# Optimization experiments

Hardware: AMD Instinct MI355X
Metric: run time of the kernel (lower is better)

The kernel has to match this reference:

```python
import jax, jax.numpy as jnp
import numpy as np

N_QUBITS = 4
N_LAYERS = 2
BATCH = 1048576


def _rx(theta):
    # PennyLane RX(theta) = exp(-i theta X / 2)
    c = jnp.cos(theta / 2).astype(jnp.complex64)
    s = jnp.sin(theta / 2).astype(jnp.complex64)
    return jnp.stack([jnp.stack([c, -1j * s]), jnp.stack([-1j * s, c])])


def _rot(phi, theta, omega):
    # PennyLane Rot(phi, theta, omega) = RZ(omega) RY(theta) RZ(phi)
    ct = jnp.cos(theta / 2)
    st = jnp.sin(theta / 2)
    e1 = jnp.exp(-0.5j * (phi + omega))
    e2 = jnp.exp(0.5j * (phi - omega))
    e3 = jnp.exp(-0.5j * (phi - omega))
    e4 = jnp.exp(0.5j * (phi + omega))
    return jnp.stack([jnp.stack([e1 * ct, -e2 * st]),
                      jnp.stack([e3 * st, e4 * ct])]).astype(jnp.complex64)


def _apply_1q(psi, U, w):
    # psi: (2,)*N_QUBITS complex statevector; contract U on wire w
    psi = jnp.tensordot(U, psi, axes=([1], [w]))
    return jnp.moveaxis(psi, 0, w)


def _apply_cnot(psi, c, t):
    psi = jnp.moveaxis(psi, (c, t), (0, 1))
    psi = jnp.stack([psi[0], psi[1, ::-1]], axis=0)  # flip target where control=1
    return jnp.moveaxis(psi, (0, 1), (c, t))


def _circuit(x, weights):
    psi = jnp.zeros((2,) * N_QUBITS, jnp.complex64).at[(0,) * N_QUBITS].set(1.0)
    # AngleEmbedding: RX(x[i]) on each wire
    for w in range(N_QUBITS):
        psi = _apply_1q(psi, _rx(x[w]), w)
    # StronglyEntanglingLayers: Rot per wire, then CNOT ring with range r
    for l in range(N_LAYERS):
        for w in range(N_QUBITS):
            psi = _apply_1q(psi, _rot(weights[l, w, 0], weights[l, w, 1], weights[l, w, 2]), w)
        r = (l % (N_QUBITS - 1)) + 1  # default ranges in StronglyEntanglingLayers
        for w in range(N_QUBITS):
            psi = _apply_cnot(psi, w, (w + r) % N_QUBITS)
    probs = jnp.real(psi * jnp.conj(psi))
    sign = jnp.array([1.0, -1.0], jnp.float32)
    z = [jnp.sum(probs * sign.reshape([2 if a == i else 1 for a in range(N_QUBITS)]))
         for i in range(N_QUBITS)]
    return jnp.stack(z)  # <Z_i> for each wire, shape [4]


def setup_inputs() -> dict:
    key = jax.random.key(0)
    k1, k2, k3, k4 = jax.random.split(key, 4)
    noise = jax.random.normal(k1, (BATCH, N_QUBITS), dtype=jnp.float32)
    q_weights = jax.random.normal(k2, (N_LAYERS, N_QUBITS, 3), dtype=jnp.float32) * 0.1
    W = jax.random.normal(k3, (4, N_QUBITS), dtype=jnp.float32) * 0.5
    b = jax.random.normal(k4, (4,), dtype=jnp.float32) * 0.1
    return {"noise": noise, "q_weights": q_weights, "W": W, "b": b}


def reference(noise, q_weights, W, b):
    q_out = jax.vmap(lambda x: _circuit(x, q_weights))(noise)  # [B, 4] float32
    out = q_out @ W.T + b                                      # Linear(4, 4)
    energy = jnp.abs(out[:, 0]) + 0.001
    return jnp.concatenate([energy[:, None], out[:, 1:]], axis=1)
```

## Files before the change

kernel.cpp:

```cpp
#include <hip/hip_runtime.h>
#include <math.h>


__global__ __launch_bounds__(256) void qg_precompute(
    const float* __restrict__ qw,
    const float* __restrict__ Wm,
    const float* __restrict__ bv,
    float* __restrict__ Dcoef)
{
  __shared__ float  gm[24][8];
  __shared__ float2 Ul[16][16];
  __shared__ float  wj[4][16];
  __shared__ float2 A[4][16][16];
  const int tid = threadIdx.x;

  if (tid < 24) {
    const float phi = qw[tid*3 + 0];
    const float th  = qw[tid*3 + 1];
    const float om  = qw[tid*3 + 2];
    float st, ct, sa, ca, sd, cd;
    __sincosf(0.5f*th,       &st, &ct);
    __sincosf(0.5f*(phi+om), &sa, &ca);
    __sincosf(0.5f*(phi-om), &sd, &cd);
    gm[tid][0] =  ca*ct; gm[tid][1] = -sa*ct;
    gm[tid][2] = -cd*st; gm[tid][3] = -sd*st;
    gm[tid][4] =  cd*st; gm[tid][5] = -sd*st;
    gm[tid][6] =  ca*ct; gm[tid][7] =  sa*ct;
  }
  if (tid >= 192) {
    const int j = (tid - 192) >> 4, k = tid & 15;
    float s = 0.f;
    #pragma unroll
    for (int i = 0; i < 4; ++i)
      s += Wm[j*4 + i] * (((k >> (3 - i)) & 1) ? -1.f : 1.f);
    wj[j][k] = s;
  }
  __syncthreads();

  {
    const int col = tid >> 4, row = tid & 15;
    float vr = (row == col) ? 1.f : 0.f, vi = 0.f;
    #pragma unroll
    for (int l = 0; l < 2; ++l) {
      #pragma unroll
      for (int w = 0; w < 4; ++w) {
        const int g = l*4 + w;
        const float m00r = gm[g][0], m00i = gm[g][1];
        const float m01r = gm[g][2], m01i = gm[g][3];
        const float m10r = gm[g][4], m10i = gm[g][5];
        const float m11r = gm[g][6], m11i = gm[g][7];
        const int mask = 8 >> w;
        const float pr = __shfl_xor(vr, mask);
        const float pi = __shfl_xor(vi, mask);
        float nr, ni;
        if (!(row & mask)) {
          nr = m00r*vr - m00i*vi + m01r*pr - m01i*pi;
          ni = m00r*vi + m00i*vr + m01r*pi + m01i*pr;
        } else {
          nr = m10r*pr - m10i*pi + m11r*vr - m11i*vi;
          ni = m10r*pi + m10i*pr + m11r*vi + m11i*vr;
        }
        vr = nr; vi = ni;
      }
      const int r = l + 1;
      #pragma unroll
      for (int w = 0; w < 4; ++w) {
        const int t  = (w + r) & 3;
        const int cm = 8 >> w, tm = 8 >> t;
        const float pr = __shfl_xor(vr, tm);
        const float pi = __shfl_xor(vi, tm);
        if (row & cm) { vr = pr; vi = pi; }
      }
    }
    Ul[row][col] = make_float2(vr, vi);
  }
  __syncthreads();

  {
    const int s = tid >> 4, t = tid & 15;
    float ar[4] = {0,0,0,0}, ai[4] = {0,0,0,0};
    #pragma unroll
    for (int k = 0; k < 16; ++k) {
      const float2 us = Ul[k][s], ut = Ul[k][t];
      const float pr = us.x*ut.x + us.y*ut.y;
      const float pi = us.x*ut.y - us.y*ut.x;
      #pragma unroll
      for (int j = 0; j < 4; ++j) { ar[j] += wj[j][k]*pr; ai[j] += wj[j][k]*pi; }
    }
    #pragma unroll
    for (int j = 0; j < 4; ++j) A[j][s][t] = make_float2(ar[j], ai[j]);
  }
  __syncthreads();

  for (int item = tid; item < 324; item += 256) {
    const int j = item / 81, p = item % 81;
    const int p1 = p / 27, p2 = (p / 9) % 3, p3 = (p / 3) % 3, p4 = p % 3;
    int ym = 0, ny = 0;
    if (p1 == 2) { ym |= 8; ++ny; }
    if (p2 == 2) { ym |= 4; ++ny; }
    if (p3 == 2) { ym |= 2; ++ny; }
    if (p4 == 2) { ym |= 1; ++ny; }
    float sum = 0.f;
    for (int t = 0; t < 16; ++t) {
      const int t0 = (t>>3)&1, t1 = (t>>2)&1, t2 = (t>>1)&1, t3 = t&1;
      float sgn = 1.f;
      if      (p1 == 1) sgn *= t0 ? -1.f : 1.f;
      else if (p1 == 2) sgn *= t0 ?  1.f : -1.f;
      if      (p2 == 1) sgn *= t1 ? -1.f : 1.f;
      else if (p2 == 2) sgn *= t1 ?  1.f : -1.f;
      if      (p3 == 1) sgn *= t2 ? -1.f : 1.f;
      else if (p3 == 2) sgn *= t2 ?  1.f : -1.f;
      if      (p4 == 1) sgn *= t3 ? -1.f : 1.f;
      else if (p4 == 2) sgn *= t3 ?  1.f : -1.f;
      const float2 ae = A[j][t ^ ym][t];
      const int m = ny & 3;
      const float re = (m == 0) ? ae.x : (m == 1) ? -ae.y : (m == 2) ? -ae.x : ae.y;
      sum += sgn * re;
    }
    sum *= 0.0625f;
    if (p == 0) sum += bv[j];
    Dcoef[p*4 + j] = sum;
  }
}

#define QG_CONST __attribute__((address_space(4)))

__global__ __launch_bounds__(256) void qg_main(
    const float4* __restrict__ noise,
    const float*  __restrict__ Dg,
    float4* __restrict__ out,
    int B)
{
  const QG_CONST float* D = (const QG_CONST float*)(unsigned long long)Dg;

  const int idx = blockIdx.x * 256 + threadIdx.x;
  if (idx >= B) return;

  const float4 x = noise[idx];
  float s0,c0,s1,c1,s2,c2,s3,c3;
  __sincosf(x.x, &s0, &c0);
  __sincosf(x.y, &s1, &c1);
  __sincosf(x.z, &s2, &c2);
  __sincosf(x.w, &s3, &c3);

  const float g34_1 = c3,   g34_2 = -s3,
              g34_3 = c2,   g34_4 = c2*c3,  g34_5 = -c2*s3,
              g34_6 = -s2,  g34_7 = -s2*c3, g34_8 = s2*s3;
  const float g12_1 = c1,   g12_2 = -s1,
              g12_3 = c0,   g12_4 = c0*c1,  g12_5 = -c0*s1,
              g12_6 = -s0,  g12_7 = -s0*c1, g12_8 = s0*s1;

  float h0, h1, h2, h3, acc0, acc1, acc2, acc3;

#define HT(a,b,g) {                                                  \
    const float qx = D[((a)*9+(b))*4+0], qy = D[((a)*9+(b))*4+1];    \
    const float qz = D[((a)*9+(b))*4+2], qw_ = D[((a)*9+(b))*4+3];   \
    h0 = fmaf(qx, (g), h0); h1 = fmaf(qy, (g), h1);                  \
    h2 = fmaf(qz, (g), h2); h3 = fmaf(qw_, (g), h3); }
#define HB(a) {                                                      \
    h0 = D[(a)*36+0]; h1 = D[(a)*36+1];                              \
    h2 = D[(a)*36+2]; h3 = D[(a)*36+3]; }                            \
    HT(a,1,g34_1) HT(a,2,g34_2) HT(a,3,g34_3) HT(a,4,g34_4)          \
    HT(a,5,g34_5) HT(a,6,g34_6) HT(a,7,g34_7) HT(a,8,g34_8)
#define ACC(g) { acc0 = fmaf((g), h0, acc0); acc1 = fmaf((g), h1, acc1); \
                 acc2 = fmaf((g), h2, acc2); acc3 = fmaf((g), h3, acc3); }

  HB(0) acc0 = h0; acc1 = h1; acc2 = h2; acc3 = h3;
  HB(1) ACC(g12_1)
  HB(2) ACC(g12_2)
  HB(3) ACC(g12_3)
  HB(4) ACC(g12_4)
  HB(5) ACC(g12_5)
  HB(6) ACC(g12_6)
  HB(7) ACC(g12_7)
  HB(8) ACC(g12_8)

#undef HT
#undef HB
#undef ACC

  out[idx] = make_float4(fabsf(acc0) + 0.001f, acc1, acc2, acc3);
}

extern "C" void kernel_launch(void* const* d_in, const int* in_sizes, int n_in,
                              void* d_out, int out_size, void* d_ws, size_t ws_size,
                              hipStream_t stream) {
  const float* noise = (const float*)d_in[0];
  const float* qw    = (const float*)d_in[1];
  const float* Wm    = (const float*)d_in[2];
  const float* bv    = (const float*)d_in[3];
  float* Dcoef = (float*)d_ws;
  const int B = in_sizes[0] / 4;

  hipLaunchKernelGGL(qg_precompute, dim3(1), dim3(256), 0, stream, qw, Wm, bv, Dcoef);

  const int blocks = (B + 255) / 256;
  hipLaunchKernelGGL(qg_main, dim3(blocks), dim3(256), 0, stream,
                     (const float4*)noise, (const float*)Dcoef, (float4*)d_out, B);
}
```

Measured before the change: 24.83 us.

## Split output channels across wavefronts with register-resident coefficients and LDS transpose

Dcoef is now stored channel-major. Each wavefront of the main kernel handles one output channel and keeps that channel's 81 coefficients in registers. Each wave evaluates 4 sample groups per iteration, and the per-channel results are transposed through shared memory so stores stay float4-coalesced. Each block covers 512 samples, which halves the grid. This removes the repeated scalar constant loads and the 4x redundant FMA chains per sample. In exchange, sincos is now computed 4x redundantly (once per wave), the kernel adds barriers and LDS traffic, and register pressure rises.

```diff
diff --git a/kernel.cpp b/kernel.cpp
--- a/kernel.cpp
+++ b/kernel.cpp
@@ -119,7 +119,7 @@
     }
     sum *= 0.0625f;
     if (p == 0) sum += bv[j];
-    Dcoef[p*4 + j] = sum;
+    Dcoef[item] = sum;
   }
 }
 
@@ -131,55 +131,74 @@
     float4* __restrict__ out,
     int B)
 {
-  const QG_CONST float* D = (const QG_CONST float*)(unsigned long long)Dg;
-
-  const int idx = blockIdx.x * 256 + threadIdx.x;
-  if (idx >= B) return;
-
-  const float4 x = noise[idx];
-  float s0,c0,s1,c1,s2,c2,s3,c3;
-  __sincosf(x.x, &s0, &c0);
-  __sincosf(x.y, &s1, &c1);
-  __sincosf(x.z, &s2, &c2);
-  __sincosf(x.w, &s3, &c3);
-
-  const float g34_1 = c3,   g34_2 = -s3,
-              g34_3 = c2,   g34_4 = c2*c3,  g34_5 = -c2*s3,
-              g34_6 = -s2,  g34_7 = -s2*c3, g34_8 = s2*s3;
-  const float g12_1 = c1,   g12_2 = -s1,
-              g12_3 = c0,   g12_4 = c0*c1,  g12_5 = -c0*s1,
-              g12_6 = -s0,  g12_7 = -s0*c1, g12_8 = s0*s1;
-
-  float h0, h1, h2, h3, acc0, acc1, acc2, acc3;
-
-#define HT(a,b,g) {                                                  \
-    const float qx = D[((a)*9+(b))*4+0], qy = D[((a)*9+(b))*4+1];    \
-    const float qz = D[((a)*9+(b))*4+2], qw_ = D[((a)*9+(b))*4+3];   \
-    h0 = fmaf(qx, (g), h0); h1 = fmaf(qy, (g), h1);                  \
-    h2 = fmaf(qz, (g), h2); h3 = fmaf(qw_, (g), h3); }
-#define HB(a) {                                                      \
-    h0 = D[(a)*36+0]; h1 = D[(a)*36+1];                              \
-    h2 = D[(a)*36+2]; h3 = D[(a)*36+3]; }                            \
-    HT(a,1,g34_1) HT(a,2,g34_2) HT(a,3,g34_3) HT(a,4,g34_4)          \
-    HT(a,5,g34_5) HT(a,6,g34_6) HT(a,7,g34_7) HT(a,8,g34_8)
-#define ACC(g) { acc0 = fmaf((g), h0, acc0); acc1 = fmaf((g), h1, acc1); \
-                 acc2 = fmaf((g), h2, acc2); acc3 = fmaf((g), h3, acc3); }
-
-  HB(0) acc0 = h0; acc1 = h1; acc2 = h2; acc3 = h3;
-  HB(1) ACC(g12_1)
-  HB(2) ACC(g12_2)
-  HB(3) ACC(g12_3)
-  HB(4) ACC(g12_4)
-  HB(5) ACC(g12_5)
-  HB(6) ACC(g12_6)
-  HB(7) ACC(g12_7)
-  HB(8) ACC(g12_8)
-
-#undef HT
-#undef HB
-#undef ACC
-
-  out[idx] = make_float4(fabsf(acc0) + 0.001f, acc1, acc2, acc3);
+  __shared__ float tr[256][4];
+
+  const int tid  = threadIdx.x;
+  const int wv   = tid >> 6;
+  const int lane = tid & 63;
+
+  const QG_CONST float* Dj =
+      ((const QG_CONST float*)(unsigned long long)Dg) + wv * 81;
+  float q[81];
+  #pragma unroll
+  for (int i = 0; i < 81; ++i) q[i] = Dj[i];
+
+  const int Bm1 = B - 1;
+
+  int base = blockIdx.x * 512;
+  #pragma unroll
+  for (int it = 0; it < 2; ++it, base += 256) {
+    #pragma unroll
+    for (int s = 0; s < 4; ++s) {
+      const int e = base + s*64 + lane;
+      const float4 x = noise[min(e, Bm1)];
+      float s0,c0,s1,c1,s2,c2,s3,c3;
+      __sincosf(x.x, &s0, &c0);
+      __sincosf(x.y, &s1, &c1);
+      __sincosf(x.z, &s2, &c2);
+      __sincosf(x.w, &s3, &c3);
+
+      const float g34_1 =  c3,     g34_2 = -s3,
+                  g34_3 =  c2,     g34_4 =  c2*c3,  g34_5 = -c2*s3,
+                  g34_6 = -s2,     g34_7 = -s2*c3,  g34_8 =  s2*s3;
+      const float g12_1 =  c1,     g12_2 = -s1,
+                  g12_3 =  c0,     g12_4 =  c0*c1,  g12_5 = -c0*s1,
+                  g12_6 = -s0,     g12_7 = -s0*c1,  g12_8 =  s0*s1;
+
+      float acc, h;
+#define ABLK(a) {                               \
+      h = q[(a)*9];                             \
+      h = fmaf(q[(a)*9+1], g34_1, h);           \
+      h = fmaf(q[(a)*9+2], g34_2, h);           \
+      h = fmaf(q[(a)*9+3], g34_3, h);           \
+      h = fmaf(q[(a)*9+4], g34_4, h);           \
+      h = fmaf(q[(a)*9+5], g34_5, h);           \
+      h = fmaf(q[(a)*9+6], g34_6, h);           \
+      h = fmaf(q[(a)*9+7], g34_7, h);           \
+      h = fmaf(q[(a)*9+8], g34_8, h); }
+
+      ABLK(0) acc = h;
+      ABLK(1) acc = fmaf(g12_1, h, acc);
+      ABLK(2) acc = fmaf(g12_2, h, acc);
+      ABLK(3) acc = fmaf(g12_3, h, acc);
+      ABLK(4) acc = fmaf(g12_4, h, acc);
+      ABLK(5) acc = fmaf(g12_5, h, acc);
+      ABLK(6) acc = fmaf(g12_6, h, acc);
+      ABLK(7) acc = fmaf(g12_7, h, acc);
+      ABLK(8) acc = fmaf(g12_8, h, acc);
+#undef ABLK
+
+      if (wv == 0) acc = fabsf(acc) + 0.001f;
+      tr[s*64 + lane][wv] = acc;
+    }
+    __syncthreads();
+    {
+      const int e = base + tid;
+      const float4 o = *(const float4*)tr[tid];
+      if (e < B) out[e] = o;
+    }
+    __syncthreads();
+  }
 }
 
 extern "C" void kernel_launch(void* const* d_in, const int* in_sizes, int n_in,
@@ -194,7 +213,7 @@
 
   hipLaunchKernelGGL(qg_precompute, dim3(1), dim3(256), 0, stream, qw, Wm, bv, Dcoef);
 
-  const int blocks = (B + 255) / 256;
+  const int blocks = (B + 511) / 512;
   hipLaunchKernelGGL(qg_main, dim3(blocks), dim3(256), 0, stream,
                      (const float4*)noise, (const float*)Dcoef, (float4*)d_out, B);
 }
```

After: 27.99 us. 12.7% more time.
